# Kernel optimization log

Hardware: AMD Instinct MI355X
Metric: run time of the kernel (lower is better)

The kernel has to match this reference:

```python
import jax, jax.numpy as jnp
import numpy as np

D_MODEL = 1024
N_HEADS = 16
HEAD_DIM = D_MODEL // N_HEADS
INNER = 4 * D_MODEL  # mlp_ratio=4
EPS = 1e-5


def setup_inputs() -> dict:
    key = jax.random.key(0)
    ks = jax.random.split(key, 8)
    B, L = 2, 2048
    s = 0.02
    return {
        "x": jax.random.normal(ks[0], (B, L, D_MODEL), dtype=jnp.float32),
        "w_qkv": jax.random.normal(ks[1], (D_MODEL, 3 * D_MODEL), dtype=jnp.float32) * s,
        "b_qkv": jnp.zeros((3 * D_MODEL,), jnp.float32),
        "w_out": jax.random.normal(ks[2], (D_MODEL, D_MODEL), dtype=jnp.float32) * s,
        "b_out": jnp.zeros((D_MODEL,), jnp.float32),
        "w_fc1": jax.random.normal(ks[3], (D_MODEL, INNER), dtype=jnp.float32) * s,
        "b_fc1": jnp.zeros((INNER,), jnp.float32),
        "w_fc2": jax.random.normal(ks[4], (INNER, D_MODEL), dtype=jnp.float32) * s,
        "b_fc2": jnp.zeros((D_MODEL,), jnp.float32),
        "ln1_g": jnp.ones((D_MODEL,), jnp.float32),
        "ln1_b": jnp.zeros((D_MODEL,), jnp.float32),
        "ln2_g": jnp.ones((D_MODEL,), jnp.float32),
        "ln2_b": jnp.zeros((D_MODEL,), jnp.float32),
    }


def _layernorm(x, g, b):
    mu = jnp.mean(x, axis=-1, keepdims=True)
    var = jnp.mean(jnp.square(x - mu), axis=-1, keepdims=True)
    return (x - mu) * jax.lax.rsqrt(var + EPS) * g + b


def reference(x, w_qkv, b_qkv, w_out, b_out, w_fc1, b_fc1, w_fc2, b_fc2,
              ln1_g, ln1_b, ln2_g, ln2_b):
    B, L, D = x.shape
    scale = HEAD_DIM ** -0.5

    # --- attention (prefill, kv_cache=None, S=L) ---
    h = _layernorm(x, ln1_g, ln1_b)
    qkv = (h @ w_qkv + b_qkv).reshape(B, L, 3, N_HEADS, HEAD_DIM)
    q, k, v = (qkv[:, :, i].transpose(0, 2, 1, 3) for i in range(3))  # (B,H,L,hd)
    attn = jnp.einsum('bhqd,bhkd->bhqk', q, k) * scale
    causal = jnp.arange(L)[None, :] > jnp.arange(L)[:, None]  # col > row
    attn = jnp.where(causal[None, None], -jnp.inf, attn)
    attn = jax.nn.softmax(attn, axis=-1)
    o = jnp.einsum('bhqk,bhkd->bhqd', attn, v).transpose(0, 2, 1, 3).reshape(B, L, D)
    x = x + o @ w_out + b_out

    # --- MLP ---
    h2 = _layernorm(x, ln2_g, ln2_b)
    h2 = jax.nn.gelu(h2 @ w_fc1 + b_fc1, approximate=False)  # torch nn.GELU = exact erf
    x = x + h2 @ w_fc2 + b_fc2
    return x
```

## Files before the change

### kernel.cpp

```cpp
#include <hip/hip_runtime.h>
#include <hip/hip_bf16.h>

typedef unsigned short u16;
typedef unsigned int u32;
typedef short bf16x8 __attribute__((ext_vector_type(8)));
typedef float f32x4 __attribute__((ext_vector_type(4)));

#define SEQ 2048
#define DM 1024
#define NH 16
#define HD 64
#define INNER 4096
#define MTOT 4096
#define QKV_ELEMS 4194304

static __device__ __forceinline__ u16 f2bf(float f) {
  u32 u = __float_as_uint(f);
  u = (u + 0x7fffu + ((u >> 16) & 1u)) >> 16;
  return (u16)u;
}

static __device__ __forceinline__ void async_copy16(void* lds, const void* g) {
  __builtin_amdgcn_global_load_lds(
      (const __attribute__((address_space(1))) u32*)g,
      (__attribute__((address_space(3))) u32*)lds, 16, 0, 0);
}

#define MFMA16(a, b, c) __builtin_amdgcn_mfma_f32_16x16x32_bf16(a, b, c, 0, 0, 0)

__global__ __launch_bounds__(256) void transpose_cast(
    const float* __restrict__ src, u16* __restrict__ dst, int K, int N) {
  __shared__ float tile[32][33];
  int bx = blockIdx.x;
  int by = blockIdx.y;
  int t = threadIdx.x;
  int tr = t >> 5, tc = t & 31;
#pragma unroll
  for (int i = 0; i < 4; ++i) {
    int r = by * 32 + tr + i * 8;
    int c = bx * 32 + tc;
    tile[tr + i * 8][tc] = src[(size_t)r * N + c];
  }
  __syncthreads();
#pragma unroll
  for (int i = 0; i < 4; ++i) {
    int n = bx * 32 + tr + i * 8;
    int kk = by * 32 + tc;
    dst[(size_t)n * K + kk] = f2bf(tile[tc][tr + i * 8]);
  }
}

__global__ __launch_bounds__(256) void ln_kernel(
    const float* __restrict__ x, const float* __restrict__ g,
    const float* __restrict__ b, u16* __restrict__ out) {
  int row = blockIdx.x, t = threadIdx.x;
  const float* xr = x + (size_t)row * DM;
  float4 v = *(const float4*)(xr + t * 4);
  float s = v.x + v.y + v.z + v.w;
  float ss = v.x * v.x + v.y * v.y + v.z * v.z + v.w * v.w;
#pragma unroll
  for (int d = 1; d < 64; d <<= 1) {
    s += __shfl_xor(s, d);
    ss += __shfl_xor(ss, d);
  }
  __shared__ float red[8];
  int w = t >> 6, lane = t & 63;
  if (lane == 0) { red[w] = s; red[4 + w] = ss; }
  __syncthreads();
  s = red[0] + red[1] + red[2] + red[3];
  ss = red[4] + red[5] + red[6] + red[7];
  float mu = s * (1.f / DM);
  float var = ss * (1.f / DM) - mu * mu;
  float rstd = rsqrtf(var + 1e-5f);
  float4 gv = *(const float4*)(g + t * 4);
  float4 bv = *(const float4*)(b + t * 4);
  u32 p0 = (u32)f2bf((v.x - mu) * rstd * gv.x + bv.x) |
           ((u32)f2bf((v.y - mu) * rstd * gv.y + bv.y) << 16);
  u32 p1 = (u32)f2bf((v.z - mu) * rstd * gv.z + bv.z) |
           ((u32)f2bf((v.w - mu) * rstd * gv.w + bv.w) << 16);
  uint2 pk; pk.x = p0; pk.y = p1;
  *(uint2*)(out + (size_t)row * DM + t * 4) = pk;
}

template <int EPI, int BN>
__global__ __launch_bounds__(256) void gemm_bt(
    const u16* __restrict__ A, const u16* __restrict__ Bt,
    const float* __restrict__ bias, const float* __restrict__ resid,
    void* __restrict__ outp, int M, int N, int K) {
  constexpr int NF = BN / 32;
  __shared__ u16 As[2][128 * 32];
  __shared__ u16 Bs[2][BN * 32];
  int t = threadIdx.x;
  int lane = t & 63, w = t >> 6;
  int lo = lane & 15, hi = lane >> 4;
  int wr = w >> 1, wc = w & 1;
  int m0 = blockIdx.y * 128, n0 = blockIdx.x * BN;

  f32x4 acc[4][NF];
#pragma unroll
  for (int i = 0; i < 4; ++i)
#pragma unroll
    for (int j = 0; j < NF; ++j) acc[i][j] = f32x4{0.f, 0.f, 0.f, 0.f};

  const u16* gA = A + (size_t)(m0 + (t >> 2)) * K + (t & 3) * 8;
  const u16* gB = Bt + (size_t)(n0 + (t >> 2)) * K + (t & 3) * 8;

  auto STAGE = [&](int buf, int kt) {
    char* lA = (char*)(&As[buf][0]) + w * 1024;
    char* lB = (char*)(&Bs[buf][0]) + w * 1024;
    async_copy16(lA, gA + kt * 32);
    async_copy16(lA + 4096, gA + (size_t)64 * K + kt * 32);
    async_copy16(lB, gB + kt * 32);
    if constexpr (BN == 128)
      async_copy16(lB + 4096, gB + (size_t)64 * K + kt * 32);
  };

  int nk = K >> 5;
  int buf = 0;
  STAGE(0, 0);
  __syncthreads();

  for (int kt = 0; kt < nk; ++kt) {
    if (kt + 1 < nk) STAGE(buf ^ 1, kt + 1);
    bf16x8 af[4], bq[NF];
#pragma unroll
    for (int f = 0; f < 4; ++f)
      af[f] = *(const bf16x8*)(&As[buf][(wr * 64 + f * 16 + lo) * 32 + hi * 8]);
#pragma unroll
    for (int j = 0; j < NF; ++j)
      bq[j] = *(const bf16x8*)(&Bs[buf][(wc * (BN / 2) + j * 16 + lo) * 32 + hi * 8]);
#pragma unroll
    for (int i = 0; i < 4; ++i)
#pragma unroll
      for (int j = 0; j < NF; ++j)
        acc[i][j] = MFMA16(af[i], bq[j], acc[i][j]);
    __syncthreads();
    buf ^= 1;
  }

#pragma unroll
  for (int i = 0; i < 4; ++i) {
#pragma unroll
    for (int j = 0; j < NF; ++j) {
      int col = n0 + wc * (BN / 2) + j * 16 + lo;
#pragma unroll
      for (int r = 0; r < 4; ++r) {
        int m = m0 + wr * 64 + i * 16 + hi * 4 + r;
        float val = acc[i][j][r];
        if constexpr (EPI == 0) {
          val += bias[col];
          int which = col >> 10;
          int h = (col >> 6) & 15, d = col & 63;
          int b = m >> 11, l = m & 2047;
          size_t bh = (size_t)(b * NH + h);
          u16* qp = (u16*)outp;
          if (which == 0)
            qp[(bh * SEQ + l) * HD + d] = f2bf(val * 0.18033688011112043f);
          else if (which == 1)
            (qp + QKV_ELEMS)[(bh * SEQ + l) * HD + d] = f2bf(val);
          else
            (qp + 2 * QKV_ELEMS)[(bh * HD + d) * SEQ + l] = f2bf(val);
        } else if constexpr (EPI == 1) {
          val += bias[col] + resid[(size_t)m * N + col];
          ((float*)outp)[(size_t)m * N + col] = val;
        } else {
          val += bias[col];
          val = 0.5f * val * (1.0f + erff(val * 0.7071067811865476f));
          ((u16*)outp)[(size_t)m * N + col] = f2bf(val);
        }
      }
    }
  }
}

__global__ __launch_bounds__(256) void attn_kernel(
    const u16* __restrict__ q, const u16* __restrict__ k,
    const u16* __restrict__ vt, u16* __restrict__ o) {
  int bx = blockIdx.x, bh = blockIdx.y;
  int t = threadIdx.x;
  int lane = t & 63, w = t >> 6;
  int lo = lane & 15, hi = lane >> 4;

  __shared__ u16 Ks[64 * 64];
  __shared__ u16 Vs[64 * 64];
  __shared__ u16 Ps[4][16][72];

  const u16* kg = k + (size_t)bh * SEQ * HD;
  const u16* vg = vt + (size_t)bh * HD * SEQ;
  int b = bh >> 4, h = bh & 15;

  u32 sw = (u32)((lo & 7) << 4);

#pragma unroll 1
  for (int pass = 0; pass < 2; ++pass) {
    int qt = pass == 0 ? (31 - bx) : bx;

    int qrow = qt * 64 + w * 16 + lo;
    const u16* qbase = q + ((size_t)bh * SEQ + qrow) * HD;
    bf16x8 qf0 = *(const bf16x8*)(qbase + hi * 8);
    bf16x8 qf1 = *(const bf16x8*)(qbase + 32 + hi * 8);

    f32x4 o_acc[4];
#pragma unroll
    for (int df = 0; df < 4; ++df) o_acc[df] = f32x4{0.f, 0.f, 0.f, 0.f};
    float m_run[4] = {-INFINITY, -INFINITY, -INFINITY, -INFINITY};
    float s_run[4] = {0.f, 0.f, 0.f, 0.f};

    for (int kt = 0; kt <= qt; ++kt) {
      __syncthreads();
#pragma unroll
      for (int p = 0; p < 2; ++p) {
        int idx = p * 256 + t;
        int r = idx >> 3, c8 = (idx & 7) * 8;
        u32 off = (u32)(r * 128 + c8 * 2);
        u32 soff = off ^ (u32)((r & 7) << 4);
        *(bf16x8*)((char*)Ks + soff) =
            *(const bf16x8*)(kg + ((size_t)(kt * 64 + r)) * HD + c8);
        *(bf16x8*)((char*)Vs + soff) =
            *(const bf16x8*)(vg + (size_t)r * SEQ + kt * 64 + c8);
      }
      __syncthreads();

      f32x4 s[4];
#pragma unroll
      for (int cf = 0; cf < 4; ++cf) {
        s[cf] = f32x4{0.f, 0.f, 0.f, 0.f};
        u32 ro = (u32)((cf * 16 + lo) * 128);
        bf16x8 kf0 = *(const bf16x8*)((char*)Ks + ((ro + hi * 16) ^ sw));
        bf16x8 kf1 = *(const bf16x8*)((char*)Ks + ((ro + 64 + hi * 16) ^ sw));
        s[cf] = MFMA16(qf0, kf0, s[cf]);
        s[cf] = MFMA16(qf1, kf1, s[cf]);
      }

      if (kt == qt) {
#pragma unroll
        for (int cf = 0; cf < 4; ++cf)
#pragma unroll
          for (int r = 0; r < 4; ++r) {
            int kcol = kt * 64 + cf * 16 + lo;
            int qr = qt * 64 + w * 16 + hi * 4 + r;
            if (kcol > qr) s[cf][r] = -INFINITY;
          }
      }

      float alpha[4];
#pragma unroll
      for (int r = 0; r < 4; ++r) {
        float v = fmaxf(fmaxf(s[0][r], s[1][r]), fmaxf(s[2][r], s[3][r]));
        v = fmaxf(v, __shfl_xor(v, 1));
        v = fmaxf(v, __shfl_xor(v, 2));
        v = fmaxf(v, __shfl_xor(v, 4));
        v = fmaxf(v, __shfl_xor(v, 8));
        float mnew = fmaxf(m_run[r], v);
        float a = exp2f(m_run[r] - mnew);
        m_run[r] = mnew;
        float psum = 0.f;
#pragma unroll
        for (int cf = 0; cf < 4; ++cf) {
          float p = exp2f(s[cf][r] - mnew);
          Ps[w][hi * 4 + r][cf * 16 + lo] = f2bf(p);
          psum += p;
        }
        psum += __shfl_xor(psum, 1);
        psum += __shfl_xor(psum, 2);
        psum += __shfl_xor(psum, 4);
        psum += __shfl_xor(psum, 8);
        s_run[r] = s_run[r] * a + psum;
        alpha[r] = a;
      }
#pragma unroll
      for (int df = 0; df < 4; ++df)
#pragma unroll
        for (int r = 0; r < 4; ++r) o_acc[df][r] *= alpha[r];

#pragma unroll
      for (int ks = 0; ks < 2; ++ks) {
        bf16x8 pf = *(const bf16x8*)&Ps[w][lo][ks * 32 + hi * 8];
#pragma unroll
        for (int df = 0; df < 4; ++df) {
          u32 ro = (u32)((df * 16 + lo) * 128);
          bf16x8 vf =
              *(const bf16x8*)((char*)Vs + ((ro + ks * 64 + hi * 16) ^ sw));
          o_acc[df] = MFMA16(pf, vf, o_acc[df]);
        }
      }
    }

#pragma unroll
    for (int df = 0; df < 4; ++df) {
#pragma unroll
      for (int r = 0; r < 4; ++r) {
        float val = o_acc[df][r] / s_run[r];
        int orow = qt * 64 + w * 16 + hi * 4 + r;
        size_t oidx = ((size_t)b * SEQ + orow) * DM + h * HD + df * 16 + lo;
        o[oidx] = f2bf(val);
      }
    }
  }
}

extern "C" void kernel_launch(void* const* d_in, const int* in_sizes, int n_in,
                              void* d_out, int out_size, void* d_ws,
                              size_t ws_size, hipStream_t stream) {
  const float* x = (const float*)d_in[0];
  const float* w_qkv = (const float*)d_in[1];
  const float* b_qkv = (const float*)d_in[2];
  const float* w_out = (const float*)d_in[3];
  const float* b_out = (const float*)d_in[4];
  const float* w_fc1 = (const float*)d_in[5];
  const float* b_fc1 = (const float*)d_in[6];
  const float* w_fc2 = (const float*)d_in[7];
  const float* b_fc2 = (const float*)d_in[8];
  const float* ln1_g = (const float*)d_in[9];
  const float* ln1_b = (const float*)d_in[10];
  const float* ln2_g = (const float*)d_in[11];
  const float* ln2_b = (const float*)d_in[12];
  float* out = (float*)d_out;

  char* ws = (char*)d_ws;
  const size_t MB = 1u << 20;
  u16* hb = (u16*)(ws + 0);
  u16* wqkvT = (u16*)(ws + 8 * MB);
  u16* woutT = (u16*)(ws + 14 * MB);
  u16* wfc1T = (u16*)(ws + 16 * MB);
  u16* wfc2T = (u16*)(ws + 24 * MB);
  u16* qb = (u16*)(ws + 32 * MB);
  u16* attn_o = (u16*)(ws + 56 * MB);
  float* x1 = (float*)(ws + 64 * MB);
  u16* gbuf = (u16*)(ws + 32 * MB);

  dim3 blk(256);

  transpose_cast<<<dim3(3072 / 32, 1024 / 32), blk, 0, stream>>>(w_qkv, wqkvT, 1024, 3072);
  transpose_cast<<<dim3(1024 / 32, 1024 / 32), blk, 0, stream>>>(w_out, woutT, 1024, 1024);
  transpose_cast<<<dim3(4096 / 32, 1024 / 32), blk, 0, stream>>>(w_fc1, wfc1T, 1024, 4096);
  transpose_cast<<<dim3(1024 / 32, 4096 / 32), blk, 0, stream>>>(w_fc2, wfc2T, 4096, 1024);

  ln_kernel<<<MTOT, blk, 0, stream>>>(x, ln1_g, ln1_b, hb);

  gemm_bt<0, 128><<<dim3(3072 / 128, MTOT / 128), blk, 0, stream>>>(
      hb, wqkvT, b_qkv, nullptr, qb, MTOT, 3072, 1024);

  attn_kernel<<<dim3(16, 32), blk, 0, stream>>>(
      qb, qb + QKV_ELEMS, qb + 2 * QKV_ELEMS, attn_o);

  gemm_bt<1, 64><<<dim3(1024 / 64, MTOT / 128), blk, 0, stream>>>(
      attn_o, woutT, b_out, x, x1, MTOT, 1024, 1024);

  ln_kernel<<<MTOT, blk, 0, stream>>>(x1, ln2_g, ln2_b, hb);

  gemm_bt<2, 128><<<dim3(4096 / 128, MTOT / 128), blk, 0, stream>>>(
      hb, wfc1T, b_fc1, nullptr, gbuf, MTOT, 4096, 1024);

  gemm_bt<1, 64><<<dim3(1024 / 64, MTOT / 128), blk, 0, stream>>>(
      gbuf, wfc2T, b_fc2, x1, out, MTOT, 1024, 4096);
}
```

Baseline: 430.6 us.

## Double-buffer attention K/V tiles with async LDS copies and lazy rescaling

```diff
diff --git a/kernel.cpp b/kernel.cpp
--- a/kernel.cpp
+++ b/kernel.cpp
@@ -181,15 +181,29 @@
   int lane = t & 63, w = t >> 6;
   int lo = lane & 15, hi = lane >> 4;
 
-  __shared__ u16 Ks[64 * 64];
-  __shared__ u16 Vs[64 * 64];
-  __shared__ u16 Ps[4][16][72];
-
-  const u16* kg = k + (size_t)bh * SEQ * HD;
-  const u16* vg = vt + (size_t)bh * HD * SEQ;
+  __shared__ u16 Ks[2][4096];
+  __shared__ u16 Vs[2][4096];
+  __shared__ u16 Ps[4][1024];
+
+  const char* kg = (const char*)(k + (size_t)bh * SEQ * HD);
+  const char* vg = (const char*)(vt + (size_t)bh * HD * SEQ);
   int b = bh >> 4, h = bh & 15;
 
   u32 sw = (u32)((lo & 7) << 4);
+
+  int koff[2], voff[2];
+#pragma unroll
+  for (int p = 0; p < 2; ++p) {
+    int g = p * 256 + w * 64 + lane;
+    int r = g >> 3, c = g & 7;
+    int cs = c ^ (r & 7);
+    koff[p] = r * 128 + cs * 16;
+    voff[p] = r * 4096 + cs * 16;
+  }
+
+  bf16x8 ones;
+#pragma unroll
+  for (int i = 0; i < 8; ++i) ones[i] = (short)0x3F80;
 
 #pragma unroll 1
   for (int pass = 0; pass < 2; ++pass) {
@@ -203,31 +217,34 @@
     f32x4 o_acc[4];
 #pragma unroll
     for (int df = 0; df < 4; ++df) o_acc[df] = f32x4{0.f, 0.f, 0.f, 0.f};
+    f32x4 o_sum = f32x4{0.f, 0.f, 0.f, 0.f};
     float m_run[4] = {-INFINITY, -INFINITY, -INFINITY, -INFINITY};
-    float s_run[4] = {0.f, 0.f, 0.f, 0.f};
+
+    auto STAGE = [&](int bb, int kt) {
+#pragma unroll
+      for (int p = 0; p < 2; ++p) {
+        async_copy16((char*)&Ks[bb][0] + p * 4096 + w * 1024,
+                     kg + (size_t)kt * 8192 + koff[p]);
+        async_copy16((char*)&Vs[bb][0] + p * 4096 + w * 1024,
+                     vg + (size_t)kt * 128 + voff[p]);
+      }
+    };
+
+    int buf = 0;
+    STAGE(0, 0);
+    __syncthreads();
 
     for (int kt = 0; kt <= qt; ++kt) {
-      __syncthreads();
-#pragma unroll
-      for (int p = 0; p < 2; ++p) {
-        int idx = p * 256 + t;
-        int r = idx >> 3, c8 = (idx & 7) * 8;
-        u32 off = (u32)(r * 128 + c8 * 2);
-        u32 soff = off ^ (u32)((r & 7) << 4);
-        *(bf16x8*)((char*)Ks + soff) =
-            *(const bf16x8*)(kg + ((size_t)(kt * 64 + r)) * HD + c8);
-        *(bf16x8*)((char*)Vs + soff) =
-            *(const bf16x8*)(vg + (size_t)r * SEQ + kt * 64 + c8);
-      }
-      __syncthreads();
+      if (kt < qt) STAGE(buf ^ 1, kt + 1);
 
       f32x4 s[4];
 #pragma unroll
       for (int cf = 0; cf < 4; ++cf) {
         s[cf] = f32x4{0.f, 0.f, 0.f, 0.f};
         u32 ro = (u32)((cf * 16 + lo) * 128);
-        bf16x8 kf0 = *(const bf16x8*)((char*)Ks + ((ro + hi * 16) ^ sw));
-        bf16x8 kf1 = *(const bf16x8*)((char*)Ks + ((ro + 64 + hi * 16) ^ sw));
+        bf16x8 kf0 = *(const bf16x8*)((char*)&Ks[buf][0] + ((ro + hi * 16) ^ sw));
+        bf16x8 kf1 =
+            *(const bf16x8*)((char*)&Ks[buf][0] + ((ro + 64 + hi * 16) ^ sw));
         s[cf] = MFMA16(qf0, kf0, s[cf]);
         s[cf] = MFMA16(qf1, kf1, s[cf]);
       }
@@ -243,7 +260,7 @@
           }
       }
 
-      float alpha[4];
+      float pmax[4];
 #pragma unroll
       for (int r = 0; r < 4; ++r) {
         float v = fmaxf(fmaxf(s[0][r], s[1][r]), fmaxf(s[2][r], s[3][r]));
@@ -251,46 +268,59 @@
         v = fmaxf(v, __shfl_xor(v, 2));
         v = fmaxf(v, __shfl_xor(v, 4));
         v = fmaxf(v, __shfl_xor(v, 8));
-        float mnew = fmaxf(m_run[r], v);
-        float a = exp2f(m_run[r] - mnew);
-        m_run[r] = mnew;
-        float psum = 0.f;
+        pmax[r] = v;
+      }
+
+      int small = (pmax[0] <= m_run[0] + 8.f) & (pmax[1] <= m_run[1] + 8.f) &
+                  (pmax[2] <= m_run[2] + 8.f) & (pmax[3] <= m_run[3] + 8.f);
+      if (!__all(small)) {
+#pragma unroll
+        for (int r = 0; r < 4; ++r) {
+          float mnew = fmaxf(m_run[r], pmax[r]);
+          float a = exp2f(m_run[r] - mnew);
+          m_run[r] = mnew;
+          o_sum[r] *= a;
+#pragma unroll
+          for (int df = 0; df < 4; ++df) o_acc[df][r] *= a;
+        }
+      }
+
+#pragma unroll
+      for (int r = 0; r < 4; ++r) {
+        int prow = hi * 4 + r;
+        u32 pbase = (u32)(prow * 128);
+        u32 psw = (u32)((prow & 7) << 4);
 #pragma unroll
         for (int cf = 0; cf < 4; ++cf) {
-          float p = exp2f(s[cf][r] - mnew);
-          Ps[w][hi * 4 + r][cf * 16 + lo] = f2bf(p);
-          psum += p;
+          float p = exp2f(s[cf][r] - m_run[r]);
+          u32 boff = pbase + (((u32)((cf * 16 + lo) * 2)) ^ psw);
+          *(u16*)((char*)&Ps[w][0] + boff) = (u16)(__float_as_uint(p) >> 16);
         }
-        psum += __shfl_xor(psum, 1);
-        psum += __shfl_xor(psum, 2);
-        psum += __shfl_xor(psum, 4);
-        psum += __shfl_xor(psum, 8);
-        s_run[r] = s_run[r] * a + psum;
-        alpha[r] = a;
-      }
-#pragma unroll
-      for (int df = 0; df < 4; ++df)
-#pragma unroll
-        for (int r = 0; r < 4; ++r) o_acc[df][r] *= alpha[r];
+      }
 
 #pragma unroll
       for (int ks = 0; ks < 2; ++ks) {
-        bf16x8 pf = *(const bf16x8*)&Ps[w][lo][ks * 32 + hi * 8];
+        u32 rboff = (u32)(lo * 128 + (((u32)(ks * 64 + hi * 16)) ^ sw));
+        bf16x8 pf = *(const bf16x8*)((char*)&Ps[w][0] + rboff);
 #pragma unroll
         for (int df = 0; df < 4; ++df) {
           u32 ro = (u32)((df * 16 + lo) * 128);
-          bf16x8 vf =
-              *(const bf16x8*)((char*)Vs + ((ro + ks * 64 + hi * 16) ^ sw));
+          bf16x8 vf = *(const bf16x8*)((char*)&Vs[buf][0] +
+                                       ((ro + ks * 64 + hi * 16) ^ sw));
           o_acc[df] = MFMA16(pf, vf, o_acc[df]);
         }
-      }
+        o_sum = MFMA16(pf, ones, o_sum);
+      }
+
+      __syncthreads();
+      buf ^= 1;
     }
 
 #pragma unroll
     for (int df = 0; df < 4; ++df) {
 #pragma unroll
       for (int r = 0; r < 4; ++r) {
-        float val = o_acc[df][r] / s_run[r];
+        float val = o_acc[df][r] / o_sum[r];
         int orow = qt * 64 + w * 16 + hi * 4 + r;
         size_t oidx = ((size_t)b * SEQ + orow) * DM + h * HD + df * 16 + lo;
         o[oidx] = f2bf(val);
```

Result: faster. 397.3 us (-7.7%).
